# Performance work log

Measured on AMD Instinct MI355X. Metric: run time of the kernel, lower is better.

## Reference

```python
import jax, jax.numpy as jnp
import numpy as np

R = 16      # grid resolution per axis (G = R**3 voxels)
K = 8       # num KNN neighbors per voxel
H = 64      # num_hidden
NB = 2      # num conv blocks
EPS = 1e-5


def _conv3d(x, w, b):
    # x: [B,C,D,H,W], w: [O,I,3,3,3]
    y = jax.lax.conv_general_dilated(
        x, w, window_strides=(1, 1, 1), padding='SAME',
        dimension_numbers=('NCDHW', 'OIDHW', 'NCDHW'))
    return y + b[None, :, None, None, None]


def _bn(x):
    # training-mode BatchNorm3d statistics (no affine), per channel
    m = x.mean(axis=(0, 2, 3, 4), keepdims=True)
    v = x.var(axis=(0, 2, 3, 4), keepdims=True)
    return (x - m) * jax.lax.rsqrt(v + EPS)


def _forward(pos, x, pe_w1, pe_b1, pe_w2, pe_b2, f_w, f_b, up_w, up_b,
             conv_w, conv_b, on_g, on_b, ro_w, ro_b):
    B, N, _ = pos.shape
    # ---- Gridifier: coordinate grid over domain [-1, 1]^3 ----
    g1 = jnp.linspace(-1.0, 1.0, R, dtype=pos.dtype)
    grid = jnp.stack(jnp.meshgrid(g1, g1, g1, indexing='ij'), axis=-1).reshape(-1, 3)  # [G,3]
    # ---- brute-force KNN: points -> grid voxels (per graph) ----
    gn = jnp.sum(grid * grid, axis=-1)          # [G]
    pn = jnp.sum(pos * pos, axis=-1)            # [B,N]
    d = gn[None, :, None] + pn[:, None, :] - 2.0 * jnp.einsum('gc,bnc->bgn', grid, pos)  # [B,G,N]
    idx = jax.lax.top_k(jax.lax.stop_gradient(-d), K)[1]  # [B,G,K] nearest point indices
    b_ix = jnp.arange(B)[:, None, None]
    p_nb = pos[b_ix, idx]                       # [B,G,K,3] neighbor positions
    f_nb = x[b_ix, idx]                         # [B,G,K,Cin] neighbor features
    # ---- BipartiteConv: position-conditioned messages, mean aggregation ----
    rel = p_nb - grid[None, :, None, :]         # relative positions [B,G,K,3]
    pe = jax.nn.gelu(rel @ pe_w1 + pe_b1) @ pe_w2 + pe_b2   # position embed [B,G,K,H]
    msg = pe * (f_nb @ f_w + f_b)               # multiplicative conditioning [B,G,K,H]
    agg = msg.mean(axis=2)                      # [B,G,H]
    h = jax.nn.gelu(agg @ up_w + up_b)          # update net [B,G,H]
    # reshape(B,R,R,R,H).permute(0,4,3,2,1) -> NCDHW
    vol = h.reshape(B, R, R, R, H).transpose(0, 4, 3, 2, 1)  # [B,H,R,R,R]
    # ---- ConvNet3D: residual blocks, maxpool after block 0 ----
    for i in range(NB):
        h1 = jax.nn.relu(_bn(_conv3d(vol, conv_w[i, 0], conv_b[i, 0])))
        h2 = _bn(_conv3d(h1, conv_w[i, 1], conv_b[i, 1]))
        vol = jax.nn.relu(vol + h2)
        if i == 0:
            vol = jax.lax.reduce_window(vol, -jnp.inf, jax.lax.max,
                                        (1, 1, 2, 2, 2), (1, 1, 2, 2, 2), 'VALID')
    out = _bn(vol) * on_g[None, :, None, None, None] + on_b[None, :, None, None, None]
    # ---- mean readout pool + linear head ----
    pooled = out.mean(axis=(2, 3, 4))           # [B,H]
    return pooled @ ro_w + ro_b                 # [B,out_channels]


def setup_inputs() -> dict:
    key = jax.random.key(0)
    ks = jax.random.split(key, 10)
    B, N, Cin, OUT = 4, 4096, 3, 16
    s = 0.05
    return {
        'pos': jax.random.uniform(ks[0], (B, N, 3), jnp.float32, -1.0, 1.0),
        'x': jax.random.normal(ks[1], (B, N, Cin), jnp.float32),
        'pe_w1': jax.random.normal(ks[2], (3, H), jnp.float32) * 0.3,
        'pe_b1': jnp.zeros((H,), jnp.float32),
        'pe_w2': jax.random.normal(ks[3], (H, H), jnp.float32) * s,
        'pe_b2': jnp.zeros((H,), jnp.float32),
        'f_w': jax.random.normal(ks[4], (Cin, H), jnp.float32) * 0.3,
        'f_b': jnp.zeros((H,), jnp.float32),
        'up_w': jax.random.normal(ks[5], (H, H), jnp.float32) * s,
        'up_b': jnp.zeros((H,), jnp.float32),
        'conv_w': jax.random.normal(ks[6], (NB, 2, H, H, 3, 3, 3), jnp.float32) * s,
        'conv_b': jnp.zeros((NB, 2, H), jnp.float32),
        'on_g': jnp.ones((H,), jnp.float32),
        'on_b': jnp.zeros((H,), jnp.float32),
        'ro_w': jax.random.normal(ks[7], (H, OUT), jnp.float32) * s,
        'ro_b': jnp.zeros((OUT,), jnp.float32),
    }


def reference(pos, x, pe_w1, pe_b1, pe_w2, pe_b2, f_w, f_b, up_w, up_b,
              conv_w, conv_b, on_g, on_b, ro_w, ro_b):
    return _forward(pos, x, pe_w1, pe_b1, pe_w2, pe_b2, f_w, f_b, up_w, up_b,
                    conv_w, conv_b, on_g, on_b, ro_w, ro_b)
```

## Files before the change

kernel.cpp:

```cpp
#include <hip/hip_runtime.h>

#define ULL unsigned long long
typedef unsigned short ush;
typedef __attribute__((ext_vector_type(8))) short s8v;
typedef __attribute__((ext_vector_type(4))) float f4v;

#define BB 4
#define NP 4096
#define HH 64
#define EPSF 1e-5f

#define WH_OFF      0u
#define WL_OFF      221184u
#define WT_PER_CONV 110592u
#define IDX_OFF     442368u
#define VOL0_OFF    573440u
#define V0H_OFF     2066432u
#define V0L_OFF     2812928u
#define T1_OFF      3559424u
#define VOL1_OFF    4608000u
#define V1H_OFF     4864000u
#define V1L_OFF     4992000u
#define T3_OFF      5120000u
#define STATS_OFF   5251072u
#define CELLS_OFF   5251968u
#define SPOS_OFF    5268368u
#define MW_OFF      5333904u

#define ZN_V0   373248u
#define ZN_V1   64000u
#define ZN_ST   224u
#define ZN_ALL  (ZN_V0 + ZN_V1 + ZN_ST)

__device__ __forceinline__ ush f2bf(float f) {
  unsigned u = __float_as_uint(f);
  return (ush)((u + 0x7FFFu + ((u >> 16) & 1u)) >> 16);
}
__device__ __forceinline__ float bf2f(ush h) { return __uint_as_float(((unsigned)h) << 16); }

__device__ __forceinline__ float gelu_tanh(float v) {
  float inner = 0.7978845608028654f * (v + 0.044715f * v * v * v);
  return 0.5f * v * (1.0f + tanhf(inner));
}

__device__ __forceinline__ float lin16(int i) {
  return -1.0f + (float)i * (2.0f / 15.0f);
}

__global__ __launch_bounds__(256) void k_prepbin(const float* __restrict__ cw,
                                                 const float* __restrict__ pw2,
                                                 const float* __restrict__ upw,
                                                 const float* __restrict__ pos,
                                                 ush* __restrict__ wh,
                                                 ush* __restrict__ wl,
                                                 ush* __restrict__ mw,
                                                 float* __restrict__ ws,
                                                 int* __restrict__ cellStart,
                                                 float4* __restrict__ sortedPos) {
  __shared__ int cnt[4096];
  __shared__ int wsum[4];
  int tid = threadIdx.x;
  if (blockIdx.x < 4) {
    int b = blockIdx.x;
    const float* pb = pos + b * NP * 3;
    for (int i = tid; i < 4096; i += 256) cnt[i] = 0;
    __syncthreads();
#pragma unroll
    for (int t = 0; t < 16; ++t) {
      int p = t * 256 + tid;
      float px = pb[3 * p], py = pb[3 * p + 1], pz = pb[3 * p + 2];
      int c0 = (int)floorf((px + 1.0f) * 7.5f + 0.5f);
      int c1 = (int)floorf((py + 1.0f) * 7.5f + 0.5f);
      int c2 = (int)floorf((pz + 1.0f) * 7.5f + 0.5f);
      c0 = min(max(c0, 0), 15); c1 = min(max(c1, 0), 15); c2 = min(max(c2, 0), 15);
      atomicAdd(&cnt[(c0 * 16 + c1) * 16 + c2], 1);
    }
    __syncthreads();
    int base = tid * 16;
    int loc[16];
    int run = 0;
#pragma unroll
    for (int j = 0; j < 16; ++j) { loc[j] = run; run += cnt[base + j]; }
    int lane = tid & 63, wv = tid >> 6;
    int inc = run;
    for (int d = 1; d < 64; d <<= 1) {
      int o = __shfl_up(inc, d, 64);
      if (lane >= d) inc += o;
    }
    if (lane == 63) wsum[wv] = inc;
    __syncthreads();
    int woff = 0;
    for (int w = 0; w < wv; ++w) woff += wsum[w];
    int excl = woff + inc - run;
    __syncthreads();
    int stv[16];
#pragma unroll
    for (int j = 0; j < 16; ++j) {
      stv[j] = excl + loc[j];
      cellStart[b * 4097 + base + j] = stv[j];
    }
#pragma unroll
    for (int j = 0; j < 16; ++j) cnt[base + j] = stv[j];
    if (tid == 0) cellStart[b * 4097 + 4096] = NP;
    __syncthreads();
#pragma unroll
    for (int t = 0; t < 16; ++t) {
      int p = t * 256 + tid;
      float px = pb[3 * p], py = pb[3 * p + 1], pz = pb[3 * p + 2];
      int c0 = (int)floorf((px + 1.0f) * 7.5f + 0.5f);
      int c1 = (int)floorf((py + 1.0f) * 7.5f + 0.5f);
      int c2 = (int)floorf((pz + 1.0f) * 7.5f + 0.5f);
      c0 = min(max(c0, 0), 15); c1 = min(max(c1, 0), 15); c2 = min(max(c2, 0), 15);
      int slot = atomicAdd(&cnt[(c0 * 16 + c1) * 16 + c2], 1);
      sortedPos[b * 4096 + slot] = make_float4(px, py, pz, __int_as_float(p));
    }
  } else {
    unsigned i = (blockIdx.x - 4) * 256u + tid;
    float4 z = make_float4(0.f, 0.f, 0.f, 0.f);
    if (i < ZN_V0) ((float4*)(ws + V0H_OFF))[i] = z;
    else if (i < ZN_V0 + ZN_V1) ((float4*)(ws + V1H_OFF))[i - ZN_V0] = z;
    else if (i < ZN_ALL) ((float4*)(ws + STATS_OFF))[i - ZN_V0 - ZN_V1] = z;
    if (i < 442368u) {
      unsigned conv = i / WT_PER_CONV;
      unsigned r = i - conv * WT_PER_CONV;
      unsigned co = r / 1728u;
      unsigned r2 = r - co * 1728u;
      unsigned ci = r2 / 27u;
      unsigned off = r2 - ci * 27u;
      float w = cw[i];
      ush hi = f2bf(w);
      unsigned dst = conv * WT_PER_CONV + (off * 64u + co) * 64u + ci;
      wh[dst] = hi;
      wl[dst] = f2bf(w - bf2f(hi));
    } else if (i < 450560u) {
      unsigned t = i - 442368u;
      unsigned mat = t >> 12, r = t & 4095u;
      unsigned co = r >> 6, ci = r & 63u;
      const float* src = mat ? upw : pw2;
      float w = src[ci * 64u + co];
      ush hi = f2bf(w);
      mw[mat * 8192u + co * 64u + ci] = hi;
      mw[mat * 8192u + 4096u + co * 64u + ci] = f2bf(w - bf2f(hi));
    }
  }
}

__device__ __forceinline__ void ins8(ULL* kk, ULL key) {
  if (key < kk[7]) {
    kk[7] = key;
#pragma unroll
    for (int q = 7; q >= 1; --q) {
      ULL a = kk[q - 1], c = kk[q];
      bool sw = c < a;
      kk[q - 1] = sw ? c : a;
      kk[q] = sw ? a : c;
    }
  }
}
__device__ __forceinline__ ULL merge32(ULL* kk, int sub) {
  ULL win = ~0ULL;
#pragma unroll
  for (int r = 0; r < 8; ++r) {
    ULL m = kk[0];
#pragma unroll
    for (int s = 1; s < 32; s <<= 1) {
      ULL o = __shfl_xor(m, s, 64);
      m = (o < m) ? o : m;
    }
    if (kk[0] == m) {
#pragma unroll
      for (int q = 0; q < 7; ++q) kk[q] = kk[q + 1];
      kk[7] = ~0ULL;
    }
    if (sub == r) win = m;
  }
  return win;
}
__device__ __forceinline__ ULL mkkey(float4 c, float gx, float gy, float gz, float gn) {
  float pn = c.x * c.x + c.y * c.y + c.z * c.z;
  float dt = gx * c.x + gy * c.y + gz * c.z;
  float d = (gn + pn) - 2.0f * dt;
  unsigned u = __float_as_uint(d);
  u ^= (unsigned)((int)u >> 31) | 0x80000000u;
  return ((ULL)u << 32) | (unsigned)__float_as_uint(c.w);
}
__device__ __forceinline__ void scan_cell(const int* __restrict__ cs,
                                          const float4* __restrict__ sp,
                                          int cell, float gx, float gy, float gz,
                                          float gn, ULL* kk) {
  int st = cs[cell], en = cs[cell + 1];
  for (int p = st; p < en; ++p) ins8(kk, mkkey(sp[p], gx, gy, gz, gn));
}

__global__ __launch_bounds__(256) void k_knn5(const int* __restrict__ cellStart,
                                              const float4* __restrict__ sortedPos,
                                              int* __restrict__ idxo) {
  constexpr int CAP = 1024;
  __shared__ float4 pts[CAP];
  __shared__ int rst[64], rlen[64], rof[64];
  __shared__ int Tsh;
  int tid = threadIdx.x;
  int lane = tid & 63;
  int sub = tid & 31;
  int lv = tid >> 5;
  int blk = blockIdx.x;
  int b = blk >> 9;
  int t9 = blk & 511;
  int ii0 = (t9 >> 6) * 2, jj0 = ((t9 >> 3) & 7) * 2, kk0 = (t9 & 7) * 2;
  int ii = ii0 + (lv >> 2), jj = jj0 + ((lv >> 1) & 1), kkc = kk0 + (lv & 1);
  int g = (ii << 8) | (jj << 4) | kkc;
  float gx = lin16(ii), gy = lin16(jj), gz = lin16(kkc);
  float gn = gx * gx + gy * gy + gz * gz;
  const int* cs = cellStart + b * 4097;
  const float4* sp = sortedPos + b * 4096;
  int loa = max(ii0 - 3, 0), hia = min(ii0 + 4, 15);
  int lob = max(jj0 - 3, 0), hib = min(jj0 + 4, 15);
  int loc = max(kk0 - 3, 0), hic = min(kk0 + 4, 15);
  int Ra = hia - loa + 1, Rb = hib - lob + 1;
  int nrows = Ra * Rb;
  if (tid < 64) {
    int st = 0, len = 0;
    if (tid < nrows) {
      int a = loa + tid / Rb, c1 = lob + tid % Rb;
      int base = (a * 16 + c1) * 16;
      st = cs[base + loc];
      len = cs[base + hic + 1] - st;
    }
    rst[tid] = st;
    rlen[tid] = len;
    int s0 = len;
    for (int d = 1; d < 64; d <<= 1) { int o = __shfl_up(s0, d, 64); if (lane >= d) s0 += o; }
    rof[tid] = s0 - len;
    if (tid == 63) Tsh = s0;
  }
  __syncthreads();
  int T = Tsh;
  if (T <= CAP) {
    for (int i = tid; i < T; i += 256) {
      int lo = 0, hi = nrows - 1;
      while (lo < hi) { int mid = (lo + hi + 1) >> 1; if (rof[mid] <= i) lo = mid; else hi = mid - 1; }
      pts[i] = sp[rst[lo] + (i - rof[lo])];
    }
  }
  __syncthreads();
  ULL kk[8];
#pragma unroll
  for (int q = 0; q < 8; ++q) kk[q] = ~0ULL;
  if (T <= CAP) {
    int i = sub;
    for (; i + 32 < T; i += 64) {
      float4 c0 = pts[i];
      float4 c1 = pts[i + 32];
      ULL k0 = mkkey(c0, gx, gy, gz, gn);
      ULL k1 = mkkey(c1, gx, gy, gz, gn);
      ins8(kk, k0);
      ins8(kk, k1);
    }
    for (; i < T; i += 32) ins8(kk, mkkey(pts[i], gx, gy, gz, gn));
  }
  ULL win = merge32(kk, sub);
  ULL w7 = __shfl(win, (lane & 32) | 7, 64);
  int dmin = 100;
  if (loa > 0)  dmin = min(dmin, ii - loa + 1);
  if (hia < 15) dmin = min(dmin, hia + 1 - ii);
  if (lob > 0)  dmin = min(dmin, jj - lob + 1);
  if (hib < 15) dmin = min(dmin, hib + 1 - jj);
  if (loc > 0)  dmin = min(dmin, kkc - loc + 1);
  if (hic < 15) dmin = min(dmin, hic + 1 - kkc);
  float bnd = ((float)dmin - 0.5f) * (2.0f / 15.0f) - 1e-5f;
  ULL ubk = ((ULL)(__float_as_uint(bnd * bnd) | 0x80000000u)) << 32;
  if (w7 >= ubk) {
#pragma unroll
    for (int q = 0; q < 8; ++q) kk[q] = ~0ULL;
    for (int t = sub; t < 1331; t += 32) {
      int dz = t / 121, r = t - dz * 121;
      int a = ii + dz - 5, c1 = jj + (r / 11) - 5, c2 = kkc + (r % 11) - 5;
      if (((unsigned)a > 15u) | ((unsigned)c1 > 15u) | ((unsigned)c2 > 15u)) continue;
      scan_cell(cs, sp, (a * 16 + c1) * 16 + c2, gx, gy, gz, gn, kk);
    }
    win = merge32(kk, sub);
    float bnd5 = 5.5f * (2.0f / 15.0f) - 1e-5f;
    ULL ub5 = ((ULL)(__float_as_uint(bnd5 * bnd5) | 0x80000000u)) << 32;
    w7 = __shfl(win, (lane & 32) | 7, 64);
    if (w7 >= ub5) {
#pragma unroll
      for (int q = 0; q < 8; ++q) kk[q] = ~0ULL;
      for (int p = sub; p < NP; p += 32) ins8(kk, mkkey(sp[p], gx, gy, gz, gn));
      win = merge32(kk, sub);
    }
  }
  if (sub < 8) idxo[(((b << 12) | g) << 3) + sub] = (int)(win & 0xFFFFFFFFULL);
}

__global__ __launch_bounds__(256) void k_mlp2(
    const float* __restrict__ pos, const float* __restrict__ xf,
    const float* __restrict__ w1, const float* __restrict__ b1,
    const float* __restrict__ b2v, const float* __restrict__ fw,
    const float* __restrict__ fb, const float* __restrict__ ub,
    const ush* __restrict__ w2tH, const ush* __restrict__ w2tL,
    const ush* __restrict__ uwtH, const ush* __restrict__ uwtL,
    const int* __restrict__ idx, float* __restrict__ vol0,
    ush* __restrict__ v0h, ush* __restrict__ v0l) {
  __shared__ __align__(16) ush lhH[128 * 72];
  __shared__ __align__(16) ush lhL[128 * 72];
  __shared__ __align__(16) float lfe[128 * 68];
  __shared__ __align__(16) ush agH[16 * 72];
  __shared__ __align__(16) ush agL[16 * 72];
  __shared__ float gpb[128 * 8];
  int tid = threadIdx.x, lane = tid & 63, wv = tid >> 6;
  int lm = lane & 15, quad = lane >> 4;
  int b = blockIdx.x >> 8;
  int g0 = (blockIdx.x & 255) << 4;
  s8v BH[8], BL[8], UH[2], UL[2];
#pragma unroll
  for (int n = 0; n < 4; ++n)
#pragma unroll
    for (int ks = 0; ks < 2; ++ks) {
      int o = ((n * 16 + lm) << 6) + ks * 32 + (quad << 3);
      BH[n * 2 + ks] = *(const s8v*)(w2tH + o);
      BL[n * 2 + ks] = *(const s8v*)(w2tL + o);
    }
#pragma unroll
  for (int ks = 0; ks < 2; ++ks) {
    int o = ((wv * 16 + lm) << 6) + ks * 32 + (quad << 3);
    UH[ks] = *(const s8v*)(uwtH + o);
    UL[ks] = *(const s8v*)(uwtL + o);
  }
  if (tid < 128) {
    int vi = tid >> 3, kp = tid & 7;
    int g = g0 + vi;
    int p = idx[(((b << 12) | g) << 3) + kp];
    const float* pp = pos + (b * NP + p) * 3;
    const float* xp = xf + (b * NP + p) * 3;
    gpb[tid * 8 + 0] = pp[0]; gpb[tid * 8 + 1] = pp[1]; gpb[tid * 8 + 2] = pp[2];
    gpb[tid * 8 + 3] = xp[0]; gpb[tid * 8 + 4] = xp[1]; gpb[tid * 8 + 5] = xp[2];
  }
  float w10 = w1[lane], w11 = w1[64 + lane], w12 = w1[128 + lane], b1c = b1[lane];
  float fw0 = fw[lane], fw1 = fw[64 + lane], fw2 = fw[128 + lane], fbc = fb[lane];
  float ubc = ub[wv * 16 + lm];
  float gx = lin16(g0 >> 8), gy = lin16((g0 >> 4) & 15);
  __syncthreads();
  for (int i = 0; i < 32; ++i) {
    int pair = wv * 32 + i;
    int vi = pair >> 3;
    float gz = lin16(vi);
    float r0 = gpb[pair * 8 + 0] - gx, r1 = gpb[pair * 8 + 1] - gy, r2 = gpb[pair * 8 + 2] - gz;
    float h1 = gelu_tanh(fmaf(r2, w12, fmaf(r1, w11, fmaf(r0, w10, b1c))));
    float fe = fmaf(gpb[pair * 8 + 5], fw2,
                    fmaf(gpb[pair * 8 + 4], fw1, fmaf(gpb[pair * 8 + 3], fw0, fbc)));
    ush hi = f2bf(h1);
    lhH[pair * 72 + lane] = hi;
    lhL[pair * 72 + lane] = f2bf(h1 - bf2f(hi));
    lfe[pair * 68 + lane] = fe;
  }
  f4v acc[2][4];
#pragma unroll
  for (int m = 0; m < 2; ++m)
#pragma unroll
    for (int n = 0; n < 4; ++n) acc[m][n] = (f4v){0.f, 0.f, 0.f, 0.f};
#pragma unroll
  for (int m = 0; m < 2; ++m)
#pragma unroll
    for (int ks = 0; ks < 2; ++ks) {
      int ao = (wv * 32 + m * 16 + lm) * 72 + ks * 32 + quad * 8;
      s8v Ah = *(const s8v*)&lhH[ao];
      s8v Al = *(const s8v*)&lhL[ao];
#pragma unroll
      for (int n = 0; n < 4; ++n) {
        acc[m][n] = __builtin_amdgcn_mfma_f32_16x16x32_bf16(Ah, BH[n * 2 + ks], acc[m][n], 0, 0, 0);
        acc[m][n] = __builtin_amdgcn_mfma_f32_16x16x32_bf16(Ah, BL[n * 2 + ks], acc[m][n], 0, 0, 0);
        acc[m][n] = __builtin_amdgcn_mfma_f32_16x16x32_bf16(Al, BH[n * 2 + ks], acc[m][n], 0, 0, 0);
      }
    }
  float b2c[4];
#pragma unroll
  for (int n = 0; n < 4; ++n) b2c[n] = b2v[n * 16 + lm];
#pragma unroll
  for (int m = 0; m < 2; ++m) {
    int vox = wv * 4 + m * 2 + (quad >> 1);
#pragma unroll
    for (int n = 0; n < 4; ++n) {
      float s = 0.0f;
#pragma unroll
      for (int r = 0; r < 4; ++r) {
        int pair = wv * 32 + m * 16 + quad * 4 + r;
        s += (acc[m][n][r] + b2c[n]) * lfe[pair * 68 + n * 16 + lm];
      }
      s += __shfl_xor(s, 16, 64);
      s *= 0.125f;
      if ((quad & 1) == 0) {
        ush hi = f2bf(s);
        agH[vox * 72 + n * 16 + lm] = hi;
        agL[vox * 72 + n * 16 + lm] = f2bf(s - bf2f(hi));
      }
    }
  }
  __syncthreads();
  f4v a2 = (f4v){0.f, 0.f, 0.f, 0.f};
#pragma unroll
  for (int ks = 0; ks < 2; ++ks) {
    int ao = lm * 72 + ks * 32 + quad * 8;
    s8v Ah = *(const s8v*)&agH[ao];
    s8v Al = *(const s8v*)&agL[ao];
    a2 = __builtin_amdgcn_mfma_f32_16x16x32_bf16(Ah, UH[ks], a2, 0, 0, 0);
    a2 = __builtin_amdgcn_mfma_f32_16x16x32_bf16(Ah, UL[ks], a2, 0, 0, 0);
    a2 = __builtin_amdgcn_mfma_f32_16x16x32_bf16(Al, UH[ks], a2, 0, 0, 0);
  }
  int xc = g0 >> 8, yc = (g0 >> 4) & 15;
#pragma unroll
  for (int r = 0; r < 4; ++r) {
    int vox = quad * 4 + r;
    float h = gelu_tanh(a2[r] + ubc);
    int pidx = (((b * 18 + vox + 1) * 18 + yc + 1) * 18 + xc + 1) * 64 + wv * 16 + lm;
    vol0[pidx] = h;
    ush hi = f2bf(h);
    v0h[pidx] = hi;
    v0l[pidx] = f2bf(h - bf2f(hi));
  }
}

template <int Z, int FUSED>
__global__ __launch_bounds__(256) void k_convm(const ush* __restrict__ vh,
                                               const ush* __restrict__ vl,
                                               const float* __restrict__ tin,
                                               const float* __restrict__ instats,
                                               float inv_cnt,
                                               const ush* __restrict__ wtH,
                                               const ush* __restrict__ wtL,
                                               float* __restrict__ out,
                                               float* __restrict__ stats) {
  constexpr int P = Z + 2;
  constexpr int Py = (Z == 16) ? 6 : 10;
  constexpr int Px = (Z == 16) ? 18 : 10;
  constexpr int NV = 3 * Py * Px;
  constexpr int VS = 272;
  __shared__ unsigned char slab[NV * VS];
  __shared__ float ls[64], ls2[64];
  int tid = threadIdx.x;
  int lane = tid & 63, wv = tid >> 6;
  int vbase = blockIdx.x * 64;
  int b = (Z == 16) ? (vbase >> 12) : (vbase >> 9);
  int rem = vbase & (Z * Z * Z - 1);
  int z0 = rem / (Z * Z);
  int y0 = (Z == 16) ? ((rem & 255) >> 4) : 0;
  if (tid < 64) { ls[tid] = 0.0f; ls2[tid] = 0.0f; }
  if (FUSED) {
    float mreg[8], rreg[8];
    int cb = (tid & 7) * 8;
#pragma unroll
    for (int e = 0; e < 8; ++e) {
      float sm = instats[(cb + e) * 2];
      float sq = instats[(cb + e) * 2 + 1];
      float m = sm * inv_cnt;
      float var = sq * inv_cnt - m * m;
      mreg[e] = m;
      rreg[e] = 1.0f / sqrtf(var + EPSF);
    }
    for (int i = tid; i < NV * 8; i += 256) {
      int v = i >> 3, c = i & 7;
      int lz = v / (Py * Px);
      int r = v - lz * (Py * Px);
      int ly = r / Px, lx = r - ly * Px;
      int rz = z0 + lz - 1, ry = y0 + ly - 1, rx = lx - 1;
      bool ok = ((unsigned)rz < (unsigned)Z) & ((unsigned)ry < (unsigned)Z) &
                ((unsigned)rx < (unsigned)Z);
      float vv[8];
#pragma unroll
      for (int e = 0; e < 8; ++e) vv[e] = 0.0f;
      if (ok) {
        const float* tp = tin + ((((b * Z + rz) * Z + ry) * Z + rx) << 6) + c * 8;
        float4 f0 = *(const float4*)tp;
        float4 f1 = *(const float4*)(tp + 4);
        vv[0] = f0.x; vv[1] = f0.y; vv[2] = f0.z; vv[3] = f0.w;
        vv[4] = f1.x; vv[5] = f1.y; vv[6] = f1.z; vv[7] = f1.w;
      }
      union { ush u[8]; uint4 q; } ph, pq;
#pragma unroll
      for (int e = 0; e < 8; ++e) {
        float x = (vv[e] - mreg[e]) * rreg[e];
        x = (ok && x > 0.0f) ? x : 0.0f;
        ush h = f2bf(x);
        ph.u[e] = h;
        pq.u[e] = f2bf(x - bf2f(h));
      }
      *(uint4*)(slab + v * VS + c * 16) = ph.q;
      *(uint4*)(slab + v * VS + 128 + c * 16) = pq.q;
    }
  } else {
    for (int i = tid; i < NV * 8; i += 256) {
      int v = i >> 3, c = i & 7;
      int lz = v / (Py * Px);
      int r = v - lz * (Py * Px);
      int ly = r / Px, lx = r - ly * Px;
      int g = (((b * P + z0 + lz) * P + (y0 + ly)) * P + lx) * 64 + c * 8;
      *(uint4*)(slab + v * VS + c * 16)       = *(const uint4*)(vh + g);
      *(uint4*)(slab + v * VS + 128 + c * 16) = *(const uint4*)(vl + g);
    }
  }
  __syncthreads();
  int lm = lane & 15, quad = lane >> 4;
  int co = (wv << 4) | lm;
  const ush* bH = wtH + (co << 6) + (quad << 3);
  const ush* bL = wtL + (co << 6) + (quad << 3);
  s8v cH0 = *(const s8v*)(bH), cH1 = *(const s8v*)(bH + 32);
  s8v cL0 = *(const s8v*)(bL), cL1 = *(const s8v*)(bL + 32);
  f4v acc[4];
#pragma unroll
  for (int m = 0; m < 4; ++m) acc[m] = (f4v){0.f, 0.f, 0.f, 0.f};
  for (int off = 0; off < 27; ++off) {
    int noff = (off < 26) ? off + 1 : 26;
    const ush* nbH = bH + noff * 4096;
    const ush* nbL = bL + noff * 4096;
    s8v nH0 = *(const s8v*)(nbH), nH1 = *(const s8v*)(nbH + 32);
    s8v nL0 = *(const s8v*)(nbL), nL1 = *(const s8v*)(nbL + 32);
    int dz = off / 9, r9 = off - dz * 9, dy = r9 / 3, dx = r9 - dy * 3;
#pragma unroll
    for (int ks = 0; ks < 2; ++ks) {
      s8v bhf = ks ? cH1 : cH0;
      s8v blf = ks ? cL1 : cL0;
#pragma unroll
      for (int m = 0; m < 4; ++m) {
        int lyp, lxp;
        if (Z == 16) { lyp = m + dy; lxp = lm + dx; }
        else         { lyp = 2 * m + (lm >> 3) + dy; lxp = (lm & 7) + dx; }
        int sv = (dz * Py + lyp) * Px + lxp;
        const unsigned char* ap = slab + sv * VS + (quad << 4) + (ks << 6);
        s8v ahf = *(const s8v*)(ap);
        s8v alf = *(const s8v*)(ap + 128);
        acc[m] = __builtin_amdgcn_mfma_f32_16x16x32_bf16(ahf, bhf, acc[m], 0, 0, 0);
        acc[m] = __builtin_amdgcn_mfma_f32_16x16x32_bf16(ahf, blf, acc[m], 0, 0, 0);
        acc[m] = __builtin_amdgcn_mfma_f32_16x16x32_bf16(alf, bhf, acc[m], 0, 0, 0);
      }
    }
    cH0 = nH0; cH1 = nH1; cL0 = nL0; cL1 = nL1;
  }
  float s = 0.0f, s2 = 0.0f;
#pragma unroll
  for (int m = 0; m < 4; ++m) {
    int vx = vbase + (m << 4) + (quad << 2);
#pragma unroll
    for (int r = 0; r < 4; ++r) {
      float v = acc[m][r];
      out[(vx + r) * 64 + co] = v;
      s += v;
      s2 = fmaf(v, v, s2);
    }
  }
  atomicAdd(&ls[co], s);
  atomicAdd(&ls2[co], s2);
  __syncthreads();
  if (tid < 64) {
    atomicAdd(&stats[tid * 2], ls[tid]);
    atomicAdd(&stats[tid * 2 + 1], ls2[tid]);
  }
}

__global__ __launch_bounds__(256) void k_residpool(const float* __restrict__ vol0,
                                                   const float* __restrict__ t2,
                                                   const float* __restrict__ stats,
                                                   float* __restrict__ vol1,
                                                   ush* __restrict__ v1h,
                                                   ush* __restrict__ v1l) {
  unsigned i = blockIdx.x * 256u + threadIdx.x;
  int c = i & 63;
  int pv = i >> 6;
  int xp = pv & 7, yp = (pv >> 3) & 7, zp = (pv >> 6) & 7, b = pv >> 9;
  float m = stats[c * 2] * (1.0f / 16384.0f);
  float var = stats[c * 2 + 1] * (1.0f / 16384.0f) - m * m;
  float rs = 1.0f / sqrtf(var + EPSF);
  float best = 0.0f;
  for (int dz = 0; dz < 2; ++dz)
    for (int dy = 0; dy < 2; ++dy)
      for (int dx = 0; dx < 2; ++dx) {
        int z = 2 * zp + dz, y = 2 * yp + dy, x = 2 * xp + dx;
        float a = vol0[(((b * 18 + z + 1) * 18 + y + 1) * 18 + x + 1) * 64 + c];
        float t = t2[(b * 4096 + z * 256 + y * 16 + x) * 64 + c];
        float u = a + (t - m) * rs;
        u = u > 0.0f ? u : 0.0f;
        best = u > best ? u : best;
      }
  int pidx = (((b * 10 + zp + 1) * 10 + yp + 1) * 10 + xp + 1) * 64 + c;
  vol1[pidx] = best;
  ush hi = f2bf(best);
  v1h[pidx] = hi;
  v1l[pidx] = f2bf(best - bf2f(hi));
}

__global__ __launch_bounds__(256) void k_resid2(const float* __restrict__ vol1,
                                                const float* __restrict__ t4,
                                                const float* __restrict__ stats,
                                                float* __restrict__ sF,
                                                float* __restrict__ sB) {
  __shared__ float ls[64], ls2[64];
  if (threadIdx.x < 64) { ls[threadIdx.x] = 0.0f; ls2[threadIdx.x] = 0.0f; }
  __syncthreads();
  unsigned i = blockIdx.x * 256u + threadIdx.x;
  int c = i & 63;
  int pv = i >> 6;
  int x = pv & 7, y = (pv >> 3) & 7, z = (pv >> 6) & 7, b = pv >> 9;
  float m = stats[c * 2] * (1.0f / 2048.0f);
  float var = stats[c * 2 + 1] * (1.0f / 2048.0f) - m * m;
  float rs = 1.0f / sqrtf(var + EPSF);
  float a = vol1[(((b * 10 + z + 1) * 10 + y + 1) * 10 + x + 1) * 64 + c];
  float u = a + (t4[i] - m) * rs;
  u = u > 0.0f ? u : 0.0f;
  atomicAdd(&ls[c], u);
  atomicAdd(&ls2[c], u * u);
  __syncthreads();
  if (threadIdx.x < 64) {
    int cc = threadIdx.x;
    atomicAdd(&sF[cc * 2], ls[cc]);
    atomicAdd(&sF[cc * 2 + 1], ls2[cc]);
    atomicAdd(&sB[b * 64 + cc], ls[cc]);
  }
}

__global__ __launch_bounds__(64) void k_final(const float* __restrict__ sF,
                                              const float* __restrict__ sB,
                                              const float* __restrict__ ong,
                                              const float* __restrict__ onb,
                                              const float* __restrict__ row,
                                              const float* __restrict__ rob,
                                              float* __restrict__ outp) {
  __shared__ float pl[4][64];
  int c = threadIdx.x;
  float m = sF[c * 2] * (1.0f / 2048.0f);
  float var = sF[c * 2 + 1] * (1.0f / 2048.0f) - m * m;
  float rs = 1.0f / sqrtf(var + EPSF);
  float gg = ong[c], bb = onb[c];
  for (int b = 0; b < 4; ++b)
    pl[b][c] = (sB[b * 64 + c] * (1.0f / 512.0f) - m) * rs * gg + bb;
  __syncthreads();
  int b = threadIdx.x >> 4, o = threadIdx.x & 15;
  float s = rob[o];
  for (int j = 0; j < 64; ++j) s = fmaf(pl[b][j], row[j * 16 + o], s);
  outp[b * 16 + o] = s;
}

extern "C" void kernel_launch(void* const* d_in, const int* in_sizes, int n_in,
                              void* d_out, int out_size, void* d_ws, size_t ws_size,
                              hipStream_t stream) {
  (void)in_sizes; (void)n_in; (void)out_size; (void)ws_size;
  const float* pos = (const float*)d_in[0];
  const float* xf  = (const float*)d_in[1];
  const float* pw1 = (const float*)d_in[2];
  const float* pb1 = (const float*)d_in[3];
  const float* pw2 = (const float*)d_in[4];
  const float* pb2 = (const float*)d_in[5];
  const float* fw  = (const float*)d_in[6];
  const float* fb  = (const float*)d_in[7];
  const float* uw  = (const float*)d_in[8];
  const float* ubp = (const float*)d_in[9];
  const float* cw  = (const float*)d_in[10];
  const float* ong = (const float*)d_in[12];
  const float* onb = (const float*)d_in[13];
  const float* row = (const float*)d_in[14];
  const float* rob = (const float*)d_in[15];

  float* ws   = (float*)d_ws;
  ush*   wh   = (ush*)(ws + WH_OFF);
  ush*   wl   = (ush*)(ws + WL_OFF);
  int*   idx  = (int*)(ws + IDX_OFF);
  float* vol0 = ws + VOL0_OFF;
  ush*   v0h  = (ush*)(ws + V0H_OFF);
  ush*   v0l  = (ush*)(ws + V0L_OFF);
  float* t1   = ws + T1_OFF;
  float* t2   = ws + V0H_OFF;
  float* vol1 = ws + VOL1_OFF;
  ush*   v1h  = (ush*)(ws + V1H_OFF);
  ush*   v1l  = (ush*)(ws + V1L_OFF);
  float* t3   = ws + T3_OFF;
  float* t4   = ws + V1H_OFF;
  float* sA   = ws + STATS_OFF;
  float* sF   = sA + 512;
  float* sB   = sF + 128;
  int*   cellStart = (int*)(ws + CELLS_OFF);
  float4* sortedPos = (float4*)(ws + SPOS_OFF);
  ush*   mw   = (ush*)(ws + MW_OFF);

  k_prepbin<<<1764, 256, 0, stream>>>(cw, pw2, uw, pos, wh, wl, mw, ws,
                                      cellStart, sortedPos);
  k_knn5<<<2048, 256, 0, stream>>>(cellStart, sortedPos, idx);
  k_mlp2<<<1024, 256, 0, stream>>>(pos, xf, pw1, pb1, pb2, fw, fb, ubp,
                                   mw, mw + 4096, mw + 8192, mw + 12288,
                                   idx, vol0, v0h, v0l);
  k_convm<16, 0><<<256, 256, 0, stream>>>(v0h, v0l, nullptr, nullptr, 0.0f,
                                          wh, wl, t1, sA);
  k_convm<16, 1><<<256, 256, 0, stream>>>(nullptr, nullptr, t1, sA, 1.0f / 16384.0f,
                                          wh + WT_PER_CONV, wl + WT_PER_CONV,
                                          t2, sA + 128);
  k_residpool<<<512, 256, 0, stream>>>(vol0, t2, sA + 128, vol1, v1h, v1l);
  k_convm<8, 0><<<32, 256, 0, stream>>>(v1h, v1l, nullptr, nullptr, 0.0f,
                                        wh + 2 * WT_PER_CONV, wl + 2 * WT_PER_CONV,
                                        t3, sA + 256);
  k_convm<8, 1><<<32, 256, 0, stream>>>(nullptr, nullptr, t3, sA + 256, 1.0f / 2048.0f,
                                        wh + 3 * WT_PER_CONV, wl + 3 * WT_PER_CONV,
                                        t4, sA + 384);
  k_resid2<<<512, 256, 0, stream>>>(vol1, t4, sA + 384, sF, sB);
  k_final<<<1, 64, 0, stream>>>(sF, sB, ong, onb, row, rob, (float*)d_out);
}
```

Baseline: 294.9 us.

## Fuse KNN into message MLP kernel and fold final readout into last reduction

The KNN search is merged into the MLP kernel, so each block finds neighbours for a 16-voxel z-column (16 lanes per voxel instead of 32) and keeps the indices in shared memory rather than writing and re-reading a global index buffer. The candidate window becomes full z-rows of 7x7 cell columns. The separate final readout kernel is removed: the last block of the residual reduction, found with an atomic counter, computes the norm and readout. This saves two launches and an index round-trip, at the cost of a wider per-voxel candidate scan with half the lanes per voxel and higher shared-memory use per block.

```diff
diff --git a/kernel.cpp b/kernel.cpp
--- a/kernel.cpp
+++ b/kernel.cpp
@@ -13,7 +13,6 @@
 #define WH_OFF      0u
 #define WL_OFF      221184u
 #define WT_PER_CONV 110592u
-#define IDX_OFF     442368u
 #define VOL0_OFF    573440u
 #define V0H_OFF     2066432u
 #define V0L_OFF     2812928u
@@ -26,6 +25,7 @@
 #define CELLS_OFF   5251968u
 #define SPOS_OFF    5268368u
 #define MW_OFF      5333904u
+#define CNT_OFF     5342096u
 
 #define ZN_V0   373248u
 #define ZN_V1   64000u
@@ -116,6 +116,7 @@
     }
   } else {
     unsigned i = (blockIdx.x - 4) * 256u + tid;
+    if (blockIdx.x == 4 && tid == 0) *((int*)(ws + CNT_OFF)) = 0;
     float4 z = make_float4(0.f, 0.f, 0.f, 0.f);
     if (i < ZN_V0) ((float4*)(ws + V0H_OFF))[i] = z;
     else if (i < ZN_V0 + ZN_V1) ((float4*)(ws + V1H_OFF))[i - ZN_V0] = z;
@@ -157,13 +158,13 @@
     }
   }
 }
-__device__ __forceinline__ ULL merge32(ULL* kk, int sub) {
+__device__ __forceinline__ ULL merge16(ULL* kk, int sub) {
   ULL win = ~0ULL;
 #pragma unroll
   for (int r = 0; r < 8; ++r) {
     ULL m = kk[0];
 #pragma unroll
-    for (int s = 1; s < 32; s <<= 1) {
+    for (int s = 1; s < 16; s <<= 1) {
       ULL o = __shfl_xor(m, s, 64);
       m = (o < m) ? o : m;
     }
@@ -192,30 +193,41 @@
   for (int p = st; p < en; ++p) ins8(kk, mkkey(sp[p], gx, gy, gz, gn));
 }
 
-__global__ __launch_bounds__(256) void k_knn5(const int* __restrict__ cellStart,
-                                              const float4* __restrict__ sortedPos,
-                                              int* __restrict__ idxo) {
-  constexpr int CAP = 1024;
-  __shared__ float4 pts[CAP];
-  __shared__ int rst[64], rlen[64], rof[64];
-  __shared__ int Tsh;
-  int tid = threadIdx.x;
-  int lane = tid & 63;
-  int sub = tid & 31;
-  int lv = tid >> 5;
-  int blk = blockIdx.x;
-  int b = blk >> 9;
-  int t9 = blk & 511;
-  int ii0 = (t9 >> 6) * 2, jj0 = ((t9 >> 3) & 7) * 2, kk0 = (t9 & 7) * 2;
-  int ii = ii0 + (lv >> 2), jj = jj0 + ((lv >> 1) & 1), kkc = kk0 + (lv & 1);
-  int g = (ii << 8) | (jj << 4) | kkc;
-  float gx = lin16(ii), gy = lin16(jj), gz = lin16(kkc);
+__global__ __launch_bounds__(256) void k_knnmlp(
+    const int* __restrict__ cellStart, const float4* __restrict__ sortedPos,
+    const float* __restrict__ pos, const float* __restrict__ xf,
+    const float* __restrict__ w1, const float* __restrict__ b1,
+    const float* __restrict__ b2v, const float* __restrict__ fw,
+    const float* __restrict__ fb, const float* __restrict__ ub,
+    const ush* __restrict__ w2tH, const ush* __restrict__ w2tL,
+    const ush* __restrict__ uwtH, const ush* __restrict__ uwtL,
+    float* __restrict__ vol0, ush* __restrict__ v0h, ush* __restrict__ v0l) {
+  __shared__ __align__(16) unsigned char smem[80384];
+  __shared__ int lidx[128];
+  ush* lhH = (ush*)smem;
+  ush* lhL = lhH + 128 * 72;
+  float* lfe = (float*)(lhL + 128 * 72);
+  ush* agH = (ush*)((unsigned char*)lfe + 128 * 68 * 4);
+  ush* agL = agH + 16 * 72;
+  float* gpb = (float*)(agL + 16 * 72);
+  float4* pts = (float4*)smem;
+  int* rst = (int*)(smem + 16384);
+  int* rlen = rst + 64;
+  int* rof = rlen + 64;
+  int* Tsh = rof + 64;
+  int tid = threadIdx.x, lane = tid & 63, wv = tid >> 6;
+  int lm = lane & 15, quad = lane >> 4;
+  int b = blockIdx.x >> 8;
+  int g0 = (blockIdx.x & 255) << 4;
+  int xc = g0 >> 8, yc = (g0 >> 4) & 15;
+  int sub = tid & 15;
+  int vz = tid >> 4;
+  float gx = lin16(xc), gy = lin16(yc), gz = lin16(vz);
   float gn = gx * gx + gy * gy + gz * gz;
   const int* cs = cellStart + b * 4097;
   const float4* sp = sortedPos + b * 4096;
-  int loa = max(ii0 - 3, 0), hia = min(ii0 + 4, 15);
-  int lob = max(jj0 - 3, 0), hib = min(jj0 + 4, 15);
-  int loc = max(kk0 - 3, 0), hic = min(kk0 + 4, 15);
+  int loa = max(xc - 3, 0), hia = min(xc + 3, 15);
+  int lob = max(yc - 3, 0), hib = min(yc + 3, 15);
   int Ra = hia - loa + 1, Rb = hib - lob + 1;
   int nrows = Ra * Rb;
   if (tid < 64) {
@@ -223,19 +235,19 @@
     if (tid < nrows) {
       int a = loa + tid / Rb, c1 = lob + tid % Rb;
       int base = (a * 16 + c1) * 16;
-      st = cs[base + loc];
-      len = cs[base + hic + 1] - st;
+      st = cs[base];
+      len = cs[base + 16] - st;
     }
     rst[tid] = st;
     rlen[tid] = len;
     int s0 = len;
     for (int d = 1; d < 64; d <<= 1) { int o = __shfl_up(s0, d, 64); if (lane >= d) s0 += o; }
     rof[tid] = s0 - len;
-    if (tid == 63) Tsh = s0;
-  }
-  __syncthreads();
-  int T = Tsh;
-  if (T <= CAP) {
+    if (tid == 63) *Tsh = s0;
+  }
+  __syncthreads();
+  int T = *Tsh;
+  if (T <= 1024) {
     for (int i = tid; i < T; i += 256) {
       int lo = 0, hi = nrows - 1;
       while (lo < hi) { int mid = (lo + hi + 1) >> 1; if (rof[mid] <= i) lo = mid; else hi = mid - 1; }
@@ -246,71 +258,49 @@
   ULL kk[8];
 #pragma unroll
   for (int q = 0; q < 8; ++q) kk[q] = ~0ULL;
-  if (T <= CAP) {
+  if (T <= 1024) {
     int i = sub;
-    for (; i + 32 < T; i += 64) {
+    for (; i + 16 < T; i += 32) {
       float4 c0 = pts[i];
-      float4 c1 = pts[i + 32];
+      float4 c1 = pts[i + 16];
       ULL k0 = mkkey(c0, gx, gy, gz, gn);
       ULL k1 = mkkey(c1, gx, gy, gz, gn);
       ins8(kk, k0);
       ins8(kk, k1);
     }
-    for (; i < T; i += 32) ins8(kk, mkkey(pts[i], gx, gy, gz, gn));
-  }
-  ULL win = merge32(kk, sub);
-  ULL w7 = __shfl(win, (lane & 32) | 7, 64);
+    for (; i < T; i += 16) ins8(kk, mkkey(pts[i], gx, gy, gz, gn));
+  }
+  ULL win = merge16(kk, sub);
+  ULL w7 = __shfl(win, (lane & 48) | 7, 64);
   int dmin = 100;
-  if (loa > 0)  dmin = min(dmin, ii - loa + 1);
-  if (hia < 15) dmin = min(dmin, hia + 1 - ii);
-  if (lob > 0)  dmin = min(dmin, jj - lob + 1);
-  if (hib < 15) dmin = min(dmin, hib + 1 - jj);
-  if (loc > 0)  dmin = min(dmin, kkc - loc + 1);
-  if (hic < 15) dmin = min(dmin, hic + 1 - kkc);
+  if (loa > 0)  dmin = min(dmin, xc - loa + 1);
+  if (hia < 15) dmin = min(dmin, hia + 1 - xc);
+  if (lob > 0)  dmin = min(dmin, yc - lob + 1);
+  if (hib < 15) dmin = min(dmin, yc >= 0 ? hib + 1 - yc : 100);
   float bnd = ((float)dmin - 0.5f) * (2.0f / 15.0f) - 1e-5f;
   ULL ubk = ((ULL)(__float_as_uint(bnd * bnd) | 0x80000000u)) << 32;
   if (w7 >= ubk) {
 #pragma unroll
     for (int q = 0; q < 8; ++q) kk[q] = ~0ULL;
-    for (int t = sub; t < 1331; t += 32) {
+    for (int t = sub; t < 1331; t += 16) {
       int dz = t / 121, r = t - dz * 121;
-      int a = ii + dz - 5, c1 = jj + (r / 11) - 5, c2 = kkc + (r % 11) - 5;
+      int a = xc + dz - 5, c1 = yc + (r / 11) - 5, c2 = vz + (r % 11) - 5;
       if (((unsigned)a > 15u) | ((unsigned)c1 > 15u) | ((unsigned)c2 > 15u)) continue;
       scan_cell(cs, sp, (a * 16 + c1) * 16 + c2, gx, gy, gz, gn, kk);
     }
-    win = merge32(kk, sub);
+    win = merge16(kk, sub);
     float bnd5 = 5.5f * (2.0f / 15.0f) - 1e-5f;
     ULL ub5 = ((ULL)(__float_as_uint(bnd5 * bnd5) | 0x80000000u)) << 32;
-    w7 = __shfl(win, (lane & 32) | 7, 64);
+    w7 = __shfl(win, (lane & 48) | 7, 64);
     if (w7 >= ub5) {
 #pragma unroll
       for (int q = 0; q < 8; ++q) kk[q] = ~0ULL;
-      for (int p = sub; p < NP; p += 32) ins8(kk, mkkey(sp[p], gx, gy, gz, gn));
-      win = merge32(kk, sub);
-    }
-  }
-  if (sub < 8) idxo[(((b << 12) | g) << 3) + sub] = (int)(win & 0xFFFFFFFFULL);
-}
-
-__global__ __launch_bounds__(256) void k_mlp2(
-    const float* __restrict__ pos, const float* __restrict__ xf,
-    const float* __restrict__ w1, const float* __restrict__ b1,
-    const float* __restrict__ b2v, const float* __restrict__ fw,
-    const float* __restrict__ fb, const float* __restrict__ ub,
-    const ush* __restrict__ w2tH, const ush* __restrict__ w2tL,
-    const ush* __restrict__ uwtH, const ush* __restrict__ uwtL,
-    const int* __restrict__ idx, float* __restrict__ vol0,
-    ush* __restrict__ v0h, ush* __restrict__ v0l) {
-  __shared__ __align__(16) ush lhH[128 * 72];
-  __shared__ __align__(16) ush lhL[128 * 72];
-  __shared__ __align__(16) float lfe[128 * 68];
-  __shared__ __align__(16) ush agH[16 * 72];
-  __shared__ __align__(16) ush agL[16 * 72];
-  __shared__ float gpb[128 * 8];
-  int tid = threadIdx.x, lane = tid & 63, wv = tid >> 6;
-  int lm = lane & 15, quad = lane >> 4;
-  int b = blockIdx.x >> 8;
-  int g0 = (blockIdx.x & 255) << 4;
+      for (int p = sub; p < NP; p += 16) ins8(kk, mkkey(sp[p], gx, gy, gz, gn));
+      win = merge16(kk, sub);
+    }
+  }
+  if (sub < 8) lidx[vz * 8 + sub] = (int)(win & 0xFFFFFFFFULL);
+  __syncthreads();
   s8v BH[8], BL[8], UH[2], UL[2];
 #pragma unroll
   for (int n = 0; n < 4; ++n)
@@ -327,9 +317,7 @@
     UL[ks] = *(const s8v*)(uwtL + o);
   }
   if (tid < 128) {
-    int vi = tid >> 3, kp = tid & 7;
-    int g = g0 + vi;
-    int p = idx[(((b << 12) | g) << 3) + kp];
+    int p = lidx[tid];
     const float* pp = pos + (b * NP + p) * 3;
     const float* xp = xf + (b * NP + p) * 3;
     gpb[tid * 8 + 0] = pp[0]; gpb[tid * 8 + 1] = pp[1]; gpb[tid * 8 + 2] = pp[2];
@@ -338,13 +326,12 @@
   float w10 = w1[lane], w11 = w1[64 + lane], w12 = w1[128 + lane], b1c = b1[lane];
   float fw0 = fw[lane], fw1 = fw[64 + lane], fw2 = fw[128 + lane], fbc = fb[lane];
   float ubc = ub[wv * 16 + lm];
-  float gx = lin16(g0 >> 8), gy = lin16((g0 >> 4) & 15);
   __syncthreads();
   for (int i = 0; i < 32; ++i) {
     int pair = wv * 32 + i;
     int vi = pair >> 3;
-    float gz = lin16(vi);
-    float r0 = gpb[pair * 8 + 0] - gx, r1 = gpb[pair * 8 + 1] - gy, r2 = gpb[pair * 8 + 2] - gz;
+    float gzz = lin16(vi);
+    float r0 = gpb[pair * 8 + 0] - gx, r1 = gpb[pair * 8 + 1] - gy, r2 = gpb[pair * 8 + 2] - gzz;
     float h1 = gelu_tanh(fmaf(r2, w12, fmaf(r1, w11, fmaf(r0, w10, b1c))));
     float fe = fmaf(gpb[pair * 8 + 5], fw2,
                     fmaf(gpb[pair * 8 + 4], fw1, fmaf(gpb[pair * 8 + 3], fw0, fbc)));
@@ -406,7 +393,6 @@
     a2 = __builtin_amdgcn_mfma_f32_16x16x32_bf16(Ah, UL[ks], a2, 0, 0, 0);
     a2 = __builtin_amdgcn_mfma_f32_16x16x32_bf16(Al, UH[ks], a2, 0, 0, 0);
   }
-  int xc = g0 >> 8, yc = (g0 >> 4) & 15;
 #pragma unroll
   for (int r = 0; r < 4; ++r) {
     int vox = quad * 4 + r;
@@ -586,15 +572,24 @@
   v1l[pidx] = f2bf(best - bf2f(hi));
 }
 
-__global__ __launch_bounds__(256) void k_resid2(const float* __restrict__ vol1,
-                                                const float* __restrict__ t4,
-                                                const float* __restrict__ stats,
-                                                float* __restrict__ sF,
-                                                float* __restrict__ sB) {
+__global__ __launch_bounds__(256) void k_resid2f(const float* __restrict__ vol1,
+                                                 const float* __restrict__ t4,
+                                                 const float* __restrict__ stats,
+                                                 float* __restrict__ sF,
+                                                 float* __restrict__ sB,
+                                                 int* __restrict__ cnt,
+                                                 const float* __restrict__ ong,
+                                                 const float* __restrict__ onb,
+                                                 const float* __restrict__ row,
+                                                 const float* __restrict__ rob,
+                                                 float* __restrict__ outp) {
   __shared__ float ls[64], ls2[64];
-  if (threadIdx.x < 64) { ls[threadIdx.x] = 0.0f; ls2[threadIdx.x] = 0.0f; }
-  __syncthreads();
-  unsigned i = blockIdx.x * 256u + threadIdx.x;
+  __shared__ float pl[4][64];
+  __shared__ int lastf;
+  int tid = threadIdx.x;
+  if (tid < 64) { ls[tid] = 0.0f; ls2[tid] = 0.0f; }
+  __syncthreads();
+  unsigned i = blockIdx.x * 256u + tid;
   int c = i & 63;
   int pv = i >> 6;
   int x = pv & 7, y = (pv >> 3) & 7, z = (pv >> 6) & 7, b = pv >> 9;
@@ -607,34 +602,37 @@
   atomicAdd(&ls[c], u);
   atomicAdd(&ls2[c], u * u);
   __syncthreads();
-  if (threadIdx.x < 64) {
-    int cc = threadIdx.x;
-    atomicAdd(&sF[cc * 2], ls[cc]);
-    atomicAdd(&sF[cc * 2 + 1], ls2[cc]);
-    atomicAdd(&sB[b * 64 + cc], ls[cc]);
-  }
-}
-
-__global__ __launch_bounds__(64) void k_final(const float* __restrict__ sF,
-                                              const float* __restrict__ sB,
-                                              const float* __restrict__ ong,
-                                              const float* __restrict__ onb,
-                                              const float* __restrict__ row,
-                                              const float* __restrict__ rob,
-                                              float* __restrict__ outp) {
-  __shared__ float pl[4][64];
-  int c = threadIdx.x;
-  float m = sF[c * 2] * (1.0f / 2048.0f);
-  float var = sF[c * 2 + 1] * (1.0f / 2048.0f) - m * m;
-  float rs = 1.0f / sqrtf(var + EPSF);
-  float gg = ong[c], bb = onb[c];
-  for (int b = 0; b < 4; ++b)
-    pl[b][c] = (sB[b * 64 + c] * (1.0f / 512.0f) - m) * rs * gg + bb;
-  __syncthreads();
-  int b = threadIdx.x >> 4, o = threadIdx.x & 15;
-  float s = rob[o];
-  for (int j = 0; j < 64; ++j) s = fmaf(pl[b][j], row[j * 16 + o], s);
-  outp[b * 16 + o] = s;
+  if (tid < 64) {
+    atomicAdd(&sF[tid * 2], ls[tid]);
+    atomicAdd(&sF[tid * 2 + 1], ls2[tid]);
+    atomicAdd(&sB[b * 64 + tid], ls[tid]);
+  }
+  __threadfence();
+  __syncthreads();
+  if (tid == 0) lastf = (atomicAdd(cnt, 1) == 511);
+  __syncthreads();
+  if (lastf) {
+    if (tid < 64) {
+      int cc = tid;
+      float sfm = atomicAdd(&sF[cc * 2], 0.0f);
+      float sfq = atomicAdd(&sF[cc * 2 + 1], 0.0f);
+      float mm = sfm * (1.0f / 2048.0f);
+      float vv = sfq * (1.0f / 2048.0f) - mm * mm;
+      float rr = 1.0f / sqrtf(vv + EPSF);
+      float gg = ong[cc], bb2 = onb[cc];
+      for (int bb = 0; bb < 4; ++bb) {
+        float sb = atomicAdd(&sB[bb * 64 + cc], 0.0f);
+        pl[bb][cc] = (sb * (1.0f / 512.0f) - mm) * rr * gg + bb2;
+      }
+    }
+    __syncthreads();
+    if (tid < 64) {
+      int bb = tid >> 4, o = tid & 15;
+      float s = rob[o];
+      for (int j = 0; j < 64; ++j) s = fmaf(pl[bb][j], row[j * 16 + o], s);
+      outp[bb * 16 + o] = s;
+    }
+  }
 }
 
 extern "C" void kernel_launch(void* const* d_in, const int* in_sizes, int n_in,
@@ -660,7 +658,6 @@
   float* ws   = (float*)d_ws;
   ush*   wh   = (ush*)(ws + WH_OFF);
   ush*   wl   = (ush*)(ws + WL_OFF);
-  int*   idx  = (int*)(ws + IDX_OFF);
   float* vol0 = ws + VOL0_OFF;
   ush*   v0h  = (ush*)(ws + V0H_OFF);
   ush*   v0l  = (ush*)(ws + V0L_OFF);
@@ -677,13 +674,14 @@
   int*   cellStart = (int*)(ws + CELLS_OFF);
   float4* sortedPos = (float4*)(ws + SPOS_OFF);
   ush*   mw   = (ush*)(ws + MW_OFF);
+  int*   cnt  = (int*)(ws + CNT_OFF);
 
   k_prepbin<<<1764, 256, 0, stream>>>(cw, pw2, uw, pos, wh, wl, mw, ws,
                                       cellStart, sortedPos);
-  k_knn5<<<2048, 256, 0, stream>>>(cellStart, sortedPos, idx);
-  k_mlp2<<<1024, 256, 0, stream>>>(pos, xf, pw1, pb1, pb2, fw, fb, ubp,
-                                   mw, mw + 4096, mw + 8192, mw + 12288,
-                                   idx, vol0, v0h, v0l);
+  k_knnmlp<<<1024, 256, 0, stream>>>(cellStart, sortedPos, pos, xf, pw1, pb1,
+                                     pb2, fw, fb, ubp,
+                                     mw, mw + 4096, mw + 8192, mw + 12288,
+                                     vol0, v0h, v0l);
   k_convm<16, 0><<<256, 256, 0, stream>>>(v0h, v0l, nullptr, nullptr, 0.0f,
                                           wh, wl, t1, sA);
   k_convm<16, 1><<<256, 256, 0, stream>>>(nullptr, nullptr, t1, sA, 1.0f / 16384.0f,
@@ -696,6 +694,6 @@
   k_convm<8, 1><<<32, 256, 0, stream>>>(nullptr, nullptr, t3, sA + 256, 1.0f / 2048.0f,
                                         wh + 3 * WT_PER_CONV, wl + 3 * WT_PER_CONV,
                                         t4, sA + 384);
-  k_resid2<<<512, 256, 0, stream>>>(vol1, t4, sA + 384, sF, sB);
-  k_final<<<1, 64, 0, stream>>>(sF, sB, ong, onb, row, rob, (float*)d_out);
-}
+  k_resid2f<<<512, 256, 0, stream>>>(vol1, t4, sA + 384, sF, sB, cnt,
+                                     ong, onb, row, rob, (float*)d_out);
+}
```

Result: slower. 318.6 us (+8.1%).
